# Performance work log

Measured on AMD Instinct MI355X. Metric: run time of the kernel, lower is better.

Reference implementation:

```python
import jax, jax.numpy as jnp
import numpy as np

N_ATOMS = 10000
N_PAIRS = 320000
C = 64        # channel width (pp_nodes[-1], ii_nodes[-1], pi_nodes[-1])
NB = 10       # n_basis
EPS = 1e-3    # torsion-boost epsilon


def setup_inputs() -> dict:
    key = jax.random.key(0)
    ks = jax.random.split(key, 24)
    f32 = jnp.float32

    def w(k, shp):
        return jax.random.normal(k, shp, f32) / np.float32(np.sqrt(shp[0]))

    ind_2 = jax.random.randint(ks[0], (N_PAIRS, 2), 0, N_ATOMS)
    p1 = jax.random.normal(ks[1], (N_ATOMS, C), f32)
    p3 = jax.random.normal(ks[2], (N_ATOMS, 3, C), f32)
    basis = jax.random.uniform(ks[3], (N_PAIRS, NB), dtype=f32)
    d3 = jax.random.normal(ks[4], (N_PAIRS, 3), f32)
    d3 = d3 / jnp.linalg.norm(d3, axis=-1, keepdims=True)  # unit bond directions
    fc_edge = jax.random.uniform(ks[5], (N_PAIRS, 1), dtype=f32)  # cutoff in [0,1]

    return {
        'ind_2': ind_2, 'p1': p1, 'p3': p3, 'basis': basis, 'd3': d3, 'fc_edge': fc_edge,
        'pp_pre_W1': w(ks[6], (C, C)), 'pp_pre_b1': jnp.zeros((C,), f32),
        'pp_pre_W2': w(ks[7], (C, C)), 'pp_pre_b2': jnp.zeros((C,), f32),
        'pi_W': w(ks[8], (2 * C, C * NB)), 'pi_b': jnp.zeros((C * NB,), f32),
        'ii_W': w(ks[9], (C, 2 * C)),
        'pp_post_W1': w(ks[10], (2 * C, C)), 'pp_post_W2': w(ks[11], (C, C)),
        'eq_pp_W': w(ks[12], (C, C)),
        'pp1_W1': w(ks[13], (2 * C, C)), 'pp1_b1': jnp.zeros((C,), f32),
        'pp1_W2': w(ks[14], (C, 2 * C)), 'pp1_b2': jnp.zeros((2 * C,), f32),
    }


def _gc_block(ind_2, p1, p3, basis, d3, fc_edge,
              pp_pre_W1, pp_pre_b1, pp_pre_W2, pp_pre_b2,
              pi_W, pi_b, ii_W, pp_post_W1, pp_post_W2,
              eq_pp_W, pp1_W1, pp1_b1, pp1_W2, pp1_b2):
    n_atoms = p1.shape[0]
    i = ind_2[:, 0]
    j = ind_2[:, 1]

    # ---- InvarLayer ----
    # pp_pre: FF [C,C], tanh, bias
    p1_in = jnp.tanh(jnp.tanh(p1 @ pp_pre_W1 + pp_pre_b1) @ pp_pre_W2 + pp_pre_b2)
    # PILayer: concat(p1[i], p1[j]) -> Dense(C*NB) -> contract with radial basis
    pair = jnp.concatenate([p1_in[i], p1_in[j]], axis=-1)            # (P, 2C)
    h = jnp.tanh(pair @ pi_W + pi_b).reshape(-1, C, NB)              # (P, C, NB)
    i_pair = jnp.einsum('pcb,pb->pc', h, basis)                      # (P, C)
    # ii: FF [2C] (doubled for n_props=2), tanh, no bias
    i_pair = jnp.tanh(i_pair @ ii_W)                                 # (P, 2C)
    # IP: scatter-add onto receiver atom i
    p1_scat = jax.ops.segment_sum(i_pair, i, num_segments=n_atoms)   # (N, 2C)
    # pp_post: FF [C,C], tanh, no bias
    p1_new = jnp.tanh(jnp.tanh(p1_scat @ pp_post_W1) @ pp_post_W2)   # (N, C)

    i1a, i1b = jnp.split(i_pair, 2, axis=-1)  # chunks; rank-3 branch uses i1s[1]

    # ---- torsion boost (compute_torsion_boost_t3) ----
    v = jax.ops.segment_sum(d3 * fc_edge, i, num_segments=n_atoms)   # (N, 3)
    v_i = v[i]
    proj = jnp.sum(v_i * d3, axis=-1, keepdims=True)
    w = v_i - proj * d3                                              # perpendicular part
    w2 = jnp.sum(w * w, axis=-1, keepdims=True)
    g_deg = w2 / (w2 + (10.0 * EPS) ** 2)
    t3 = w * jax.lax.rsqrt(w2 + EPS * EPS) * g_deg                   # (P, 3)
    tb_gate = g_deg * (fc_edge * fc_edge)                            # (P, 1)

    # ---- EquivarLayer ----
    gate = i1b[:, None, :]                                           # (P, 1, C)
    ix = p3[j] * gate + d3[:, :, None] * gate \
         + t3[:, :, None] * (i1b * tb_gate)[:, None, :]              # (P, 3, C)
    p3_new = jax.ops.segment_sum(ix, i, num_segments=n_atoms)        # (N, 3, C)
    p3_new = p3_new @ eq_pp_W                                        # PP: no bias, no act
    dotted = jnp.einsum('ixr,ixr->ir', p3_new, p3_new)               # (N, C)

    # ---- output PP + gating ----
    h2 = jnp.tanh(jnp.concatenate([p1_new, dotted], axis=-1) @ pp1_W1 + pp1_b1)
    h2 = jnp.tanh(h2 @ pp1_W2 + pp1_b2)                              # (N, 2C)
    g1, g3 = jnp.split(h2, 2, axis=-1)
    p1_out = g1                                                      # (N, C)
    p3_out = p3_new * g3[:, None, :]                                 # ScaleLayer
    return p1_out, p3_out


def reference(ind_2, p1, p3, basis, d3, fc_edge,
              pp_pre_W1, pp_pre_b1, pp_pre_W2, pp_pre_b2,
              pi_W, pi_b, ii_W, pp_post_W1, pp_post_W2,
              eq_pp_W, pp1_W1, pp1_b1, pp1_W2, pp1_b2):
    return _gc_block(ind_2, p1, p3, basis, d3, fc_edge,
                     pp_pre_W1, pp_pre_b1, pp_pre_W2, pp_pre_b2,
                     pi_W, pi_b, ii_W, pp_post_W1, pp_post_W2,
                     eq_pp_W, pp1_W1, pp1_b1, pp1_W2, pp1_b2)
```

## Files before the change

kernel.cpp:

```cpp
#include <hip/hip_runtime.h>
#include <hip/hip_bf16.h>

#define N_ATOMS 10000
#define N_PAIRS 320000
#define C_ 64
#define NB_ 10

typedef short bf16x8 __attribute__((ext_vector_type(8)));
typedef float f32x4 __attribute__((ext_vector_type(4)));

__device__ __forceinline__ float bf2f(__hip_bfloat16 x) { return __bfloat162float(x); }
__device__ __forceinline__ float ldf(const void* p, int i, int isf32) {
    return isf32 ? ((const float*)p)[i] : bf2f(((const __hip_bfloat16*)p)[i]);
}
__device__ __forceinline__ short f2bs(float x) {
    __hip_bfloat16 h = __float2bfloat16(x);
    return *reinterpret_cast<short*>(&h);
}
__device__ __forceinline__ float bs2f(unsigned short s) {
    return __uint_as_float(((unsigned)s) << 16);
}
__device__ __forceinline__ float tanh_fast(float x) {
    const float e = __expf(2.0f * x);
    return 1.0f - 2.0f * __builtin_amdgcn_rcpf(e + 1.0f);
}

#define W_PPREW1 0
#define W_PPREB1 4096
#define W_PPREW2 4160
#define W_PPREB2 8256
#define W_PIW    8320
#define W_PIB    90240
#define W_IIW    90880
#define W_PPOSTW1 99072
#define W_PPOSTW2 107264
#define W_EQW    111360
#define W_Q1W    115456
#define W_Q1B    123648
#define W_Q2W    123712
#define W_Q2B    131904
#define W_TOTAL  132032

__device__ __forceinline__ int probe_eval(const void* d3)
{
    float sf = 0.f, sb = 0.f;
    const float* f = (const float*)d3;
    const __hip_bfloat16* b = (const __hip_bfloat16*)d3;
    for (int r = 0; r < 4; r++) {
        float x = f[r*3], y = f[r*3+1], z = f[r*3+2];
        float n = x*x + y*y + z*z;
        sf += isfinite(n) ? fabsf(n - 1.f) : 1e30f;
        float xb = bf2f(b[r*3]), yb = bf2f(b[r*3+1]), zb = bf2f(b[r*3+2]);
        float nb = xb*xb + yb*yb + zb*zb;
        sb += isfinite(nb) ? fabsf(nb - 1.f) : 1e30f;
    }
    return (sf < sb) ? 1 : 0;
}

__global__ __launch_bounds__(256) void k_front(
    const void* __restrict__ d3, const void* __restrict__ fc,
    int* __restrict__ flag, const int* __restrict__ ind2,
    int* __restrict__ cnt, float* __restrict__ v,
    const void* s0, const void* s1, const void* s2, const void* s3,
    const void* s4, const void* s5, const void* s6, const void* s7,
    const void* s8, const void* s9, const void* s10, const void* s11,
    const void* s12, const void* s13,
    float* __restrict__ wbuf)
{
    __shared__ int fsh;
    if (threadIdx.x == 0) {
        const int fv = probe_eval(d3);
        fsh = fv;
        if (blockIdx.x == 0) *flag = fv;
    }
    __syncthreads();
    const int isf32 = fsh;
    if (blockIdx.x < 1250) {
        const int p = blockIdx.x * 256 + threadIdx.x;
        if (p >= N_PAIRS) return;
        const int ia = ind2[2 * p];
        atomicAdd(&cnt[ia], 1);
        const float f = ldf(fc, p, isf32);
        #pragma unroll
        for (int x = 0; x < 3; x++)
            atomicAdd(&v[ia * 3 + x], ldf(d3, 3 * p + x, isf32) * f);
        return;
    }
    const int idx = (blockIdx.x - 1250) * 256 + threadIdx.x;
    if (idx >= W_TOTAL) return;
    const int offw[15] = {W_PPREW1, W_PPREB1, W_PPREW2, W_PPREB2, W_PIW, W_PIB,
                          W_IIW, W_PPOSTW1, W_PPOSTW2, W_EQW, W_Q1W, W_Q1B,
                          W_Q2W, W_Q2B, W_TOTAL};
    const void* srcs[14] = {s0,s1,s2,s3,s4,s5,s6,s7,s8,s9,s10,s11,s12,s13};
    int t = 0;
    while (idx >= offw[t + 1]) t++;
    wbuf[idx] = ldf(srcs[t], idx - offw[t], isf32);
}

__global__ __launch_bounds__(256) void k_scan_wfrag(
    const int* __restrict__ cnt, int* __restrict__ offs, int* __restrict__ cur,
    const float* __restrict__ wbuf,
    short* __restrict__ w1Fh, short* __restrict__ w1Fl,
    short* __restrict__ w2Fh, short* __restrict__ w2Fl)
{
    if (blockIdx.x == 0) {
        if (!cnt) return;
        __shared__ int part[256];
        __shared__ int base[257];
        const int t = threadIdx.x;
        const int lo = t * 40, hi = (lo + 40 < N_ATOMS) ? lo + 40 : N_ATOMS;
        int s = 0;
        for (int b = lo; b < hi; b++) s += cnt[b];
        part[t] = s;
        __syncthreads();
        if (t == 0) {
            int run = 0;
            for (int i = 0; i < 256; i++) { base[i] = run; run += part[i]; }
            base[256] = run;
        }
        __syncthreads();
        int run = base[t];
        for (int b = lo; b < hi; b++) { offs[b] = run; cur[b] = run; run += cnt[b]; }
        if (t == 0) offs[N_ATOMS] = base[256];
        return;
    }
    const int b = blockIdx.x - 1;
    const int isW2 = b >= 16;
    const int idx = (b - (isW2 ? 16 : 0)) * 256 + threadIdx.x;
    const int j = idx & 7, lane = (idx >> 3) & 63, s2 = (idx >> 9) & 1, ct = idx >> 10;
    const int k = s2 * 32 + (lane >> 4) * 8 + j;
    const int col = ct * 16 + (lane & 15);
    const float wv = wbuf[(isW2 ? W_PPREW2 : W_PPREW1) + k * 64 + col];
    const short hs = f2bs(wv);
    short* dh = isW2 ? w2Fh : w1Fh;
    short* dl = isW2 ? w2Fl : w1Fl;
    dh[idx] = hs;
    dl[idx] = f2bs(wv - bs2f((unsigned short)hs));
}

__global__ __launch_bounds__(256) void k_prep_scatter(
    const float* __restrict__ wbuf,
    short* __restrict__ piWB2,
    short* __restrict__ iiWh, short* __restrict__ iiWl,
    const void* __restrict__ p1, const int* __restrict__ flagp,
    unsigned short* __restrict__ p1h, unsigned short* __restrict__ p1l,
    const int* __restrict__ ind2, int* __restrict__ cur, int* __restrict__ perm,
    const short* __restrict__ w1Fh, const short* __restrict__ w1Fl,
    const short* __restrict__ w2Fh, const short* __restrict__ w2Fl)
{
    __shared__ float hL[64 * 68];
    if (blockIdx.x >= 509) {
        const int p = (blockIdx.x - 509) * 256 + threadIdx.x;
        if (p < N_PAIRS) {
            const int pos = atomicAdd(&cur[ind2[2 * p]], 1);
            perm[pos] = p;
        }
        return;
    }
    if (blockIdx.x < 352) {
        int idx = blockIdx.x * 256 + threadIdx.x;
        if (idx < 81920) {
            const int j = idx & 7, lane = (idx >> 3) & 63, s = (idx >> 9) & 3, T = idx >> 11;
            const int k = s * 32 + (lane >> 4) * 8 + j;
            const int colp = T * 16 + (lane & 15);
            const int b = colp >> 6, c = colp & 63;
            const float v = wbuf[W_PIW + k * 640 + c * 10 + b];
            const short hs = f2bs(v);
            const int cc = idx >> 13, e = idx & 8191;
            piWB2[cc * 16384 + e] = hs;
            piWB2[cc * 16384 + 8192 + e] = f2bs(v - bs2f((unsigned short)hs));
            return;
        }
        idx -= 81920;
        if (idx < 8192) {
            const int j = idx & 7, lane = (idx >> 3) & 63, s2 = (idx >> 9) & 1, ct = idx >> 10;
            const int k = s2 * 32 + (lane >> 4) * 8 + j;
            const int col = ct * 16 + (lane & 15);
            const float wv = wbuf[W_IIW + k * 128 + col];
            const short hs = f2bs(wv);
            iiWh[idx] = hs;
            iiWl[idx] = f2bs(wv - bs2f((unsigned short)hs));
        }
        return;
    }
    const int isf32 = *flagp;
    const int t = threadIdx.x;
    const int lane = t & 63, w = t >> 6, lc = lane & 15, quad = lane >> 4;
    const int B0 = (blockIdx.x - 352) * 64;

    bf16x8 xh[2], xl[2];
    {
        const int a = B0 + w * 16 + lc;
        const int ar = (a < N_ATOMS) ? a : N_ATOMS - 1;
        #pragma unroll
        for (int s2 = 0; s2 < 2; s2++) {
            const int base = ar * 64 + s2 * 32 + quad * 8;
            #pragma unroll
            for (int j = 0; j < 8; j++) {
                const float x = ldf(p1, base + j, isf32);
                const short hs = f2bs(x);
                xh[s2][j] = hs;
                xl[s2][j] = f2bs(x - bs2f((unsigned short)hs));
            }
        }
    }
    #pragma unroll
    for (int tt = 0; tt < 4; tt++) {
        f32x4 acc = {0.f, 0.f, 0.f, 0.f};
        #pragma unroll
        for (int s2 = 0; s2 < 2; s2++) {
            bf16x8 bh = *(const bf16x8*)&w1Fh[((tt * 2 + s2) * 64 + lane) * 8];
            bf16x8 bl = *(const bf16x8*)&w1Fl[((tt * 2 + s2) * 64 + lane) * 8];
            acc = __builtin_amdgcn_mfma_f32_16x16x32_bf16(xh[s2], bh, acc, 0, 0, 0);
            acc = __builtin_amdgcn_mfma_f32_16x16x32_bf16(xl[s2], bh, acc, 0, 0, 0);
            acc = __builtin_amdgcn_mfma_f32_16x16x32_bf16(xh[s2], bl, acc, 0, 0, 0);
        }
        const int c = tt * 16 + lc;
        const float b1v = wbuf[W_PPREB1 + c];
        #pragma unroll
        for (int r = 0; r < 4; r++) {
            const int m = w * 16 + quad * 4 + r;
            hL[m * 68 + c] = tanh_fast(acc[r] + b1v);
        }
    }
    __syncthreads();
    bf16x8 hh[2], hl[2];
    {
        const int row = w * 16 + lc;
        #pragma unroll
        for (int s2 = 0; s2 < 2; s2++) {
            const float* pr = &hL[row * 68 + s2 * 32 + quad * 8];
            #pragma unroll
            for (int j = 0; j < 8; j++) {
                const float x = pr[j];
                const short hs = f2bs(x);
                hh[s2][j] = hs;
                hl[s2][j] = f2bs(x - bs2f((unsigned short)hs));
            }
        }
    }
    #pragma unroll
    for (int tt = 0; tt < 4; tt++) {
        f32x4 acc = {0.f, 0.f, 0.f, 0.f};
        #pragma unroll
        for (int s2 = 0; s2 < 2; s2++) {
            bf16x8 bh = *(const bf16x8*)&w2Fh[((tt * 2 + s2) * 64 + lane) * 8];
            bf16x8 bl = *(const bf16x8*)&w2Fl[((tt * 2 + s2) * 64 + lane) * 8];
            acc = __builtin_amdgcn_mfma_f32_16x16x32_bf16(hh[s2], bh, acc, 0, 0, 0);
            acc = __builtin_amdgcn_mfma_f32_16x16x32_bf16(hl[s2], bh, acc, 0, 0, 0);
            acc = __builtin_amdgcn_mfma_f32_16x16x32_bf16(hh[s2], bl, acc, 0, 0, 0);
        }
        const int c = tt * 16 + lc;
        const float b2v = wbuf[W_PPREB2 + c];
        #pragma unroll
        for (int r = 0; r < 4; r++) {
            const int m = w * 16 + quad * 4 + r;
            const int a = B0 + m;
            if (a < N_ATOMS) {
                const float f = tanh_fast(acc[r] + b2v);
                const short hs = f2bs(f);
                p1h[a * 64 + c] = (unsigned short)hs;
                p1l[a * 64 + c] = (unsigned short)f2bs(f - bs2f((unsigned short)hs));
            }
        }
    }
}

__global__ __launch_bounds__(256) void k_pairs_fused(
    const int* __restrict__ ind2, const void* __restrict__ basis,
    const void* __restrict__ d3, const void* __restrict__ fc,
    const int* __restrict__ perm,
    const void* __restrict__ p3,
    const float* __restrict__ wbuf,
    const short* __restrict__ piWB2,
    const short* __restrict__ iiWh, const short* __restrict__ iiWl,
    const unsigned short* __restrict__ p1h, const unsigned short* __restrict__ p1l,
    const int* __restrict__ flagp, const float* __restrict__ vglob,
    float* __restrict__ p1scat, float* __restrict__ p3acc)
{
    __shared__ __align__(16) char SH[33280];
    __shared__ float basisL[640];
    __shared__ float biasT[640];
    __shared__ int sIL[65], sJL[64];
    __shared__ float d3L[64][3], t3L[64][3], tbL[64];

    unsigned short* Bbuf = (unsigned short*)SH;
    float* preL = (float*)SH;
    float* ipL  = (float*)SH;

    const int t = threadIdx.x;
    const int bid = blockIdx.x;
    const int P0 = ((bid & 7) * 625 + (bid >> 3)) * 64;
    const int isf32 = *flagp;
    const int lane = t & 63;
    const int w = t >> 6;
    const int lc = lane & 15;
    const int quad = lane >> 4;

    if (t < 64) {
        const int p = perm[P0 + t];
        int2 ij = ((const int2*)ind2)[p];
        sIL[t] = ij.x; sJL[t] = ij.y;
        const float vi0 = vglob[ij.x * 3 + 0], vi1 = vglob[ij.x * 3 + 1], vi2 = vglob[ij.x * 3 + 2];
        const float d0 = ldf(d3, 3 * p + 0, isf32);
        const float d1 = ldf(d3, 3 * p + 1, isf32);
        const float d2 = ldf(d3, 3 * p + 2, isf32);
        d3L[t][0] = d0; d3L[t][1] = d1; d3L[t][2] = d2;
        const float proj = vi0 * d0 + vi1 * d1 + vi2 * d2;
        const float w0 = vi0 - proj * d0, w1 = vi1 - proj * d1, w2v = vi2 - proj * d2;
        const float w2 = w0 * w0 + w1 * w1 + w2v * w2v;
        const float g = w2 / (w2 + 1e-4f);
        const float rs = rsqrtf(w2 + 1e-6f);
        t3L[t][0] = w0 * rs * g; t3L[t][1] = w1 * rs * g; t3L[t][2] = w2v * rs * g;
        const float f = ldf(fc, p, isf32);
        tbL[t] = g * f * f;
    }
    if (t == 64) sIL[64] = -1;
    for (int e = t; e < 640; e += 256) {
        const int pm = e / 10, col = e - pm * 10;
        basisL[e] = ldf(basis, perm[P0 + pm] * 10 + col, isf32);
    }
    for (int e = t; e < 640; e += 256) biasT[e] = wbuf[W_PIB + (e & 63) * 10 + (e >> 6)];
    __syncthreads();

    bf16x8 ah[4], al[4];
    {
        const int ia = sIL[w * 16 + lc];
        const int ja = sJL[w * 16 + lc];
        #pragma unroll
        for (int s = 0; s < 4; s++) {
            const int atom = (s < 2) ? ia : ja;
            const int off = atom * 64 + (s & 1) * 32 + quad * 8;
            ah[s] = *(const bf16x8*)(p1h + off);
            al[s] = *(const bf16x8*)(p1l + off);
        }
    }

    float sr[4][4];
    #pragma unroll
    for (int r = 0; r < 4; r++)
        #pragma unroll
        for (int ph = 0; ph < 4; ph++) sr[r][ph] = 0.f;

    for (int cc = 0; cc < 10; cc++) {
        if (cc) __syncthreads();
        {
            const uint4* gsrc = (const uint4*)(piWB2 + cc * 16384);
            uint4* ldst = (uint4*)Bbuf;
            #pragma unroll
            for (int r = 0; r < 8; r++) ldst[r * 256 + t] = gsrc[r * 256 + t];
        }
        __syncthreads();
        #pragma unroll
        for (int tt = 0; tt < 4; tt++) {
            f32x4 acc = {0.f, 0.f, 0.f, 0.f};
            #pragma unroll
            for (int s = 0; s < 4; s++) {
                const int e = ((tt * 4 + s) * 64 + lane) * 8;
                bf16x8 bh = *(const bf16x8*)&Bbuf[e];
                bf16x8 bl = *(const bf16x8*)&Bbuf[8192 + e];
                acc = __builtin_amdgcn_mfma_f32_16x16x32_bf16(ah[s], bh, acc, 0, 0, 0);
                acc = __builtin_amdgcn_mfma_f32_16x16x32_bf16(al[s], bh, acc, 0, 0, 0);
                acc = __builtin_amdgcn_mfma_f32_16x16x32_bf16(ah[s], bl, acc, 0, 0, 0);
            }
            const float bias = biasT[cc * 64 + tt * 16 + lc];
            #pragma unroll
            for (int r = 0; r < 4; r++) {
                const int m = w * 16 + quad * 4 + r;
                const float h = tanh_fast(acc[r] + bias);
                sr[r][tt] += h * basisL[m * 10 + cc];
            }
        }
    }
    __syncthreads();

    #pragma unroll
    for (int r = 0; r < 4; r++)
        #pragma unroll
        for (int ph = 0; ph < 4; ph++)
            preL[(w * 16 + quad * 4 + r) * 68 + ph * 16 + lc] = sr[r][ph];
    __syncthreads();

    bf16x8 ah2[2], al2[2];
    {
        const int row = w * 16 + lc;
        #pragma unroll
        for (int s2 = 0; s2 < 2; s2++) {
            const float* pr2 = &preL[row * 68 + s2 * 32 + quad * 8];
            #pragma unroll
            for (int j = 0; j < 8; j++) {
                const float x = pr2[j];
                const short hs = f2bs(x);
                ah2[s2][j] = hs;
                al2[s2][j] = f2bs(x - bs2f((unsigned short)hs));
            }
        }
    }
    __syncthreads();

    float pv0[16];
    if (t < 192) {
        #pragma unroll
        for (int u = 0; u < 16; u++) pv0[u] = ldf(p3, sJL[u] * 192 + t, isf32);
    }

    #pragma unroll
    for (int ct = 0; ct < 8; ct++) {
        f32x4 acc = {0.f, 0.f, 0.f, 0.f};
        #pragma unroll
        for (int s2 = 0; s2 < 2; s2++) {
            bf16x8 bh = *(const bf16x8*)&iiWh[((ct * 2 + s2) * 64 + lane) * 8];
            bf16x8 bl = *(const bf16x8*)&iiWl[((ct * 2 + s2) * 64 + lane) * 8];
            acc = __builtin_amdgcn_mfma_f32_16x16x32_bf16(ah2[s2], bh, acc, 0, 0, 0);
            acc = __builtin_amdgcn_mfma_f32_16x16x32_bf16(al2[s2], bh, acc, 0, 0, 0);
            acc = __builtin_amdgcn_mfma_f32_16x16x32_bf16(ah2[s2], bl, acc, 0, 0, 0);
        }
        const int ch = ct * 16 + lc;
        #pragma unroll
        for (int r = 0; r < 4; r++) {
            const int m = w * 16 + quad * 4 + r;
            ipL[m * 130 + ch] = tanh_fast(acc[r]);
        }
    }
    __syncthreads();

    if (t < 192) {
        const int x = t >> 6, cc2 = t & 63;
        float acc = 0.f;
        #pragma unroll
        for (int blk = 0; blk < 4; blk++) {
            float pv[16];
            if (blk == 0) {
                #pragma unroll
                for (int u = 0; u < 16; u++) pv[u] = pv0[u];
            } else {
                #pragma unroll
                for (int u = 0; u < 16; u++)
                    pv[u] = ldf(p3, sJL[blk * 16 + u] * 192 + t, isf32);
            }
            #pragma unroll
            for (int u = 0; u < 16; u++) {
                const int m = blk * 16 + u;
                const float ipb = ipL[m * 130 + 64 + cc2];
                acc += (pv[u] + d3L[m][x]) * ipb + t3L[m][x] * (ipb * tbL[m]);
                if (sIL[m + 1] != sIL[m]) {
                    atomicAdd(&p3acc[(size_t)sIL[m] * 192 + t], acc);
                    acc = 0.f;
                }
            }
        }
    } else {
        const int ch0 = t - 192;
        float a0 = 0.f, a1 = 0.f;
        #pragma unroll 8
        for (int m = 0; m < 64; m++) {
            a0 += ipL[m * 130 + ch0];
            a1 += ipL[m * 130 + 64 + ch0];
            if (sIL[m + 1] != sIL[m]) {
                const size_t base = (size_t)sIL[m] * 128;
                atomicAdd(&p1scat[base + ch0], a0);
                atomicAdd(&p1scat[base + 64 + ch0], a1);
                a0 = 0.f; a1 = 0.f;
            }
        }
    }
}

__global__ __launch_bounds__(256) void k_pairs_atomic(
    const int* __restrict__ ind2, const void* __restrict__ basis,
    const void* __restrict__ d3, const void* __restrict__ fc,
    const void* __restrict__ p3,
    const float* __restrict__ wbuf,
    const short* __restrict__ piWB2,
    const short* __restrict__ iiWh, const short* __restrict__ iiWl,
    const unsigned short* __restrict__ p1h, const unsigned short* __restrict__ p1l,
    const int* __restrict__ flagp, const float* __restrict__ vglob,
    float* __restrict__ outA, float* __restrict__ outB)
{
    __shared__ __align__(16) unsigned short Bbuf[8192];
    __shared__ __align__(16) char SH[17408];
    __shared__ float basisL[640];
    __shared__ int sIL[64], sJL[64];
    __shared__ float d3L[64][3], t3L[64][3], tbL[64];

    float* preL = (float*)SH;
    float* i1bL = (float*)SH;

    const int t = threadIdx.x;
    const int P0 = blockIdx.x * 64;
    const int isf32 = *flagp;
    const int lane = t & 63;
    const int w = t >> 6;
    const int lc = lane & 15;
    const int quad = lane >> 4;

    if (t < 64) {
        int2 ij = ((const int2*)ind2)[P0 + t];
        sIL[t] = ij.x; sJL[t] = ij.y;
    }
    for (int e = t; e < 640; e += 256) basisL[e] = ldf(basis, P0 * 10 + e, isf32);
    __syncthreads();

    bf16x8 ah[4], al[4];
    {
        const int ia = sIL[w * 16 + lc];
        const int ja = sJL[w * 16 + lc];
        #pragma unroll
        for (int s = 0; s < 4; s++) {
            const int atom = (s < 2) ? ia : ja;
            const int off = atom * 64 + (s & 1) * 32 + quad * 8;
            ah[s] = *(const bf16x8*)(p1h + off);
            al[s] = *(const bf16x8*)(p1l + off);
        }
    }

    float sr[4][4];
    #pragma unroll
    for (int r = 0; r < 4; r++)
        #pragma unroll
        for (int ph = 0; ph < 4; ph++) sr[r][ph] = 0.f;

    for (int cc = 0; cc < 10; cc++) {
        f32x4 acc[4];
        #pragma unroll
        for (int tt = 0; tt < 4; tt++) acc[tt] = (f32x4){0.f, 0.f, 0.f, 0.f};

        __syncthreads();
        {
            const uint4* gsrc = (const uint4*)(piWB2 + cc * 16384);
            uint4* ldst = (uint4*)Bbuf;
            #pragma unroll
            for (int r = 0; r < 4; r++) ldst[r * 256 + t] = gsrc[r * 256 + t];
        }
        __syncthreads();
        #pragma unroll
        for (int tt = 0; tt < 4; tt++) {
            #pragma unroll
            for (int s = 0; s < 4; s++) {
                bf16x8 bfr = *(const bf16x8*)&Bbuf[((tt * 4 + s) * 64 + lane) * 8];
                acc[tt] = __builtin_amdgcn_mfma_f32_16x16x32_bf16(ah[s], bfr, acc[tt], 0, 0, 0);
                acc[tt] = __builtin_amdgcn_mfma_f32_16x16x32_bf16(al[s], bfr, acc[tt], 0, 0, 0);
            }
        }
        __syncthreads();
        {
            const uint4* gsrc = (const uint4*)(piWB2 + cc * 16384 + 8192);
            uint4* ldst = (uint4*)Bbuf;
            #pragma unroll
            for (int r = 0; r < 4; r++) ldst[r * 256 + t] = gsrc[r * 256 + t];
        }
        __syncthreads();
        #pragma unroll
        for (int tt = 0; tt < 4; tt++) {
            #pragma unroll
            for (int s = 0; s < 4; s++) {
                bf16x8 bfr = *(const bf16x8*)&Bbuf[((tt * 4 + s) * 64 + lane) * 8];
                acc[tt] = __builtin_amdgcn_mfma_f32_16x16x32_bf16(ah[s], bfr, acc[tt], 0, 0, 0);
            }
            const int c = tt * 16 + lc;
            const float bias = wbuf[W_PIB + c * 10 + cc];
            #pragma unroll
            for (int r = 0; r < 4; r++) {
                const int m = w * 16 + quad * 4 + r;
                const float h = tanh_fast(acc[tt][r] + bias);
                sr[r][tt] += h * basisL[m * 10 + cc];
            }
        }
    }

    #pragma unroll
    for (int r = 0; r < 4; r++)
        #pragma unroll
        for (int ph = 0; ph < 4; ph++)
            preL[(w * 16 + quad * 4 + r) * 68 + ph * 16 + lc] = sr[r][ph];
    __syncthreads();

    bf16x8 ah2[2], al2[2];
    {
        const int row = w * 16 + lc;
        #pragma unroll
        for (int s2 = 0; s2 < 2; s2++) {
            const float* pr2 = &preL[row * 68 + s2 * 32 + quad * 8];
            #pragma unroll
            for (int j = 0; j < 8; j++) {
                const float x = pr2[j];
                const short hs = f2bs(x);
                ah2[s2][j] = hs;
                al2[s2][j] = f2bs(x - bs2f((unsigned short)hs));
            }
        }
    }
    __syncthreads();

    #pragma unroll
    for (int ct = 0; ct < 8; ct++) {
        f32x4 acc = {0.f, 0.f, 0.f, 0.f};
        #pragma unroll
        for (int s2 = 0; s2 < 2; s2++) {
            bf16x8 bh = *(const bf16x8*)&iiWh[((ct * 2 + s2) * 64 + lane) * 8];
            bf16x8 bl = *(const bf16x8*)&iiWl[((ct * 2 + s2) * 64 + lane) * 8];
            acc = __builtin_amdgcn_mfma_f32_16x16x32_bf16(ah2[s2], bh, acc, 0, 0, 0);
            acc = __builtin_amdgcn_mfma_f32_16x16x32_bf16(al2[s2], bh, acc, 0, 0, 0);
            acc = __builtin_amdgcn_mfma_f32_16x16x32_bf16(ah2[s2], bl, acc, 0, 0, 0);
        }
        const int ch = ct * 16 + lc;
        #pragma unroll
        for (int r = 0; r < 4; r++) {
            const int m = w * 16 + quad * 4 + r;
            const float val = tanh_fast(acc[r]);
            atomicAdd(&outA[(size_t)sIL[m] * 128 + ch], val);
            if (ch >= 64) i1bL[m * 64 + (ch - 64)] = val;
        }
    }

    __syncthreads();
    if (t < 64) {
        const int m = t;
        const int ia = sIL[m];
        const float vi0 = vglob[ia * 3 + 0], vi1 = vglob[ia * 3 + 1], vi2 = vglob[ia * 3 + 2];
        const float d0 = ldf(d3, (P0 + m) * 3 + 0, isf32);
        const float d1 = ldf(d3, (P0 + m) * 3 + 1, isf32);
        const float d2 = ldf(d3, (P0 + m) * 3 + 2, isf32);
        d3L[m][0] = d0; d3L[m][1] = d1; d3L[m][2] = d2;
        const float proj = vi0 * d0 + vi1 * d1 + vi2 * d2;
        const float w0 = vi0 - proj * d0, w1 = vi1 - proj * d1, w2v = vi2 - proj * d2;
        const float w2 = w0 * w0 + w1 * w1 + w2v * w2v;
        const float g = w2 / (w2 + 1e-4f);
        const float rs = rsqrtf(w2 + 1e-6f);
        t3L[m][0] = w0 * rs * g; t3L[m][1] = w1 * rs * g; t3L[m][2] = w2v * rs * g;
        const float f = ldf(fc, P0 + m, isf32);
        tbL[m] = g * f * f;
    }
    __syncthreads();
    const int c = lane;
    #pragma unroll 4
    for (int mm = 0; mm < 16; mm++) {
        const int m = w * 16 + mm;
        const float bv = i1bL[m * 64 + c];
        const float coef = bv * tbL[m];
        #pragma unroll
        for (int x = 0; x < 3; x++) {
            const float p3v = ldf(p3, sJL[m] * 192 + x * 64 + c, isf32);
            atomicAdd(&outB[(size_t)sIL[m] * 192 + x * 64 + c],
                      p3v * bv + d3L[m][x] * bv + t3L[m][x] * coef);
        }
    }
}

__global__ __launch_bounds__(256) void k_final(
    const float* __restrict__ p1scat, const float* __restrict__ p3acc,
    const float* __restrict__ wbuf, const int* __restrict__ flagp,
    void* __restrict__ out)
{
    const float* ppW1 = wbuf + W_PPOSTW1;
    const float* ppW2 = wbuf + W_PPOSTW2;
    const float* eqW  = wbuf + W_EQW;
    const float* q1W  = wbuf + W_Q1W;
    const float* q1b  = wbuf + W_Q1B;
    const float* q2W  = wbuf + W_Q2W;
    const float* q2b  = wbuf + W_Q2B;
    const int isf32 = *flagp;

    __shared__ float s1[4][128];
    __shared__ float hA[4][64];
    __shared__ float cat[4][128];
    __shared__ float p3a[4][192];
    const int t = threadIdx.x;
    const int slot = t >> 6, c = t & 63;
    const int atom = blockIdx.x * 4 + slot;

    s1[slot][c]        = p1scat[atom * 128 + c];
    s1[slot][64 + c]   = p1scat[atom * 128 + 64 + c];
    p3a[slot][c]       = p3acc[atom * 192 + c];
    p3a[slot][64 + c]  = p3acc[atom * 192 + 64 + c];
    p3a[slot][128 + c] = p3acc[atom * 192 + 128 + c];
    __syncthreads();

    float acc = 0.f;
    for (int k = 0; k < 128; k++) acc += s1[slot][k] * ppW1[k * 64 + c];
    hA[slot][c] = tanh_fast(acc);
    __syncthreads();
    acc = 0.f;
    for (int k = 0; k < 64; k++) acc += hA[slot][k] * ppW2[k * 64 + c];
    cat[slot][c] = tanh_fast(acc);

    float pn[3];
    float dot = 0.f;
    #pragma unroll
    for (int x = 0; x < 3; x++) {
        float a = 0.f;
        for (int k = 0; k < 64; k++) a += p3a[slot][x * 64 + k] * eqW[k * 64 + c];
        pn[x] = a;
        dot += a * a;
    }
    cat[slot][64 + c] = dot;
    __syncthreads();

    acc = q1b[c];
    for (int k = 0; k < 128; k++) acc += cat[slot][k] * q1W[k * 64 + c];
    __syncthreads();
    hA[slot][c] = tanh_fast(acc);
    __syncthreads();

    float g1acc = q2b[c], g3acc = q2b[c + 64];
    for (int k = 0; k < 64; k++) {
        const float hv = hA[slot][k];
        g1acc += hv * q2W[k * 128 + c];
        g3acc += hv * q2W[k * 128 + c + 64];
    }
    const float g1 = tanh_fast(g1acc);
    const float g3 = tanh_fast(g3acc);
    if (isf32) {
        float* p1o = (float*)out;
        float* p3o = p1o + 640000;
        p1o[atom * 64 + c] = g1;
        #pragma unroll
        for (int x = 0; x < 3; x++) p3o[atom * 192 + x * 64 + c] = pn[x] * g3;
    } else {
        __hip_bfloat16* p1o = (__hip_bfloat16*)out;
        __hip_bfloat16* p3o = p1o + 640000;
        p1o[atom * 64 + c] = __float2bfloat16(g1);
        #pragma unroll
        for (int x = 0; x < 3; x++) p3o[atom * 192 + x * 64 + c] = __float2bfloat16(pn[x] * g3);
    }
}

extern "C" void kernel_launch(void* const* d_in, const int* in_sizes, int n_in,
                              void* d_out, int out_size, void* d_ws, size_t ws_size,
                              hipStream_t stream)
{
    const int* ind2 = (const int*)d_in[0];
    const void* p1    = d_in[1];
    const void* p3    = d_in[2];
    const void* basis = d_in[3];
    const void* d3    = d_in[4];
    const void* fc    = d_in[5];

    char* W = (char*)d_ws;
    float* wbuf  = (float*)(W + 0);
    short* piWB2 = (short*)(W + 528128);
    short* iiWh  = (short*)(W + 1183488);
    short* iiWl  = (short*)(W + 1199872);
    unsigned short* p1h = (unsigned short*)(W + 1216256);
    unsigned short* p1l = (unsigned short*)(W + 2496256);
    int* flag = (int*)(W + 3776256);
    short* w1Fh = (short*)(W + 3776320);
    short* w1Fl = (short*)(W + 3784512);
    short* w2Fh = (short*)(W + 3792704);
    short* w2Fl = (short*)(W + 3800896);

    const int fused = (ws_size >= 18129216ULL) ? 1 : 0;

    if (fused) {
        int* offs     = (int*)(W + 3809088);
        int* cur      = (int*)(W + 3849216);
        int* perm     = (int*)(W + 3889216);
        int* cnt      = (int*)(W + 5169216);
        float* v      = (float*)(W + 5209216);
        float* p1scat = (float*)(W + 5329216);
        float* p3acc  = (float*)(W + 10449216);

        hipMemsetAsync(cnt, 0, 40000 + 120000 + 5120000 + 7680000, stream);
        k_front<<<1766, 256, 0, stream>>>(d3, fc, flag, ind2, cnt, v,
            d_in[6], d_in[7], d_in[8], d_in[9], d_in[10], d_in[11], d_in[12],
            d_in[13], d_in[14], d_in[15], d_in[16], d_in[17], d_in[18], d_in[19],
            wbuf);
        k_scan_wfrag<<<33, 256, 0, stream>>>(cnt, offs, cur, wbuf,
                                             w1Fh, w1Fl, w2Fh, w2Fl);
        k_prep_scatter<<<1759, 256, 0, stream>>>(wbuf, piWB2, iiWh, iiWl, p1, flag,
                                                 p1h, p1l, ind2, cur, perm,
                                                 w1Fh, w1Fl, w2Fh, w2Fl);
        k_pairs_fused<<<5000, 256, 0, stream>>>(ind2, basis, d3, fc, perm, p3,
                                                wbuf, piWB2, iiWh, iiWl,
                                                p1h, p1l, flag, v, p1scat, p3acc);
        k_final<<<2500, 256, 0, stream>>>(p1scat, p3acc, wbuf, flag, d_out);
    } else {
        int* cnt      = (int*)(W + 3809088);
        float* v      = (float*)(W + 3849088);
        float* p1scat = (float*)(W + 3969088);
        float* p3acc  = (float*)(W + 9089088);

        hipMemsetAsync(cnt, 0, 40000 + 120000 + 5120000 + 7680000, stream);
        k_front<<<1766, 256, 0, stream>>>(d3, fc, flag, ind2, cnt, v,
            d_in[6], d_in[7], d_in[8], d_in[9], d_in[10], d_in[11], d_in[12],
            d_in[13], d_in[14], d_in[15], d_in[16], d_in[17], d_in[18], d_in[19],
            wbuf);
        k_scan_wfrag<<<33, 256, 0, stream>>>(nullptr, nullptr, nullptr, wbuf,
                                             w1Fh, w1Fl, w2Fh, w2Fl);
        k_prep_scatter<<<509, 256, 0, stream>>>(wbuf, piWB2, iiWh, iiWl, p1, flag,
                                                p1h, p1l, nullptr, nullptr, nullptr,
                                                w1Fh, w1Fl, w2Fh, w2Fl);
        k_pairs_atomic<<<5000, 256, 0, stream>>>(ind2, basis, d3, fc, p3,
                                                 wbuf, piWB2, iiWh, iiWl,
                                                 p1h, p1l, flag, v,
                                                 p1scat, p3acc);
        k_final<<<2500, 256, 0, stream>>>(p1scat, p3acc, wbuf, flag, d_out);
    }
}
```

Before: 522.8 us.

## Rewrite per-atom output MLP as split-bf16 MFMA kernel with prepacked weight fragments

Replaces the scalar per-atom final kernel, which handled 4 atoms per block, with an MFMA kernel that handles 64 atoms per block. Every dense layer (pp_post, eq_pp, pp1) uses hi/lo bf16 splitting with three MFMAs to stay close to fp32 accuracy. The scan kernel gains extra blocks that pack those weights into MFMA fragment layout, and workspace offsets are shifted to make room. The aim is to cut the FMA-bound cost of the final stage, at the price of three MFMAs per product, a larger prep launch and a bigger workspace requirement.

```diff
diff --git a/kernel.cpp b/kernel.cpp
--- a/kernel.cpp
+++ b/kernel.cpp
@@ -101,16 +101,22 @@
     const int* __restrict__ cnt, int* __restrict__ offs, int* __restrict__ cur,
     const float* __restrict__ wbuf,
     short* __restrict__ w1Fh, short* __restrict__ w1Fl,
-    short* __restrict__ w2Fh, short* __restrict__ w2Fl)
+    short* __restrict__ w2Fh, short* __restrict__ w2Fl,
+    short* __restrict__ pAh, short* __restrict__ pAl,
+    short* __restrict__ pBh, short* __restrict__ pBl,
+    short* __restrict__ pEh, short* __restrict__ pEl,
+    short* __restrict__ pQ1h, short* __restrict__ pQ1l,
+    short* __restrict__ pQ2h, short* __restrict__ pQ2l)
 {
-    if (blockIdx.x == 0) {
+    const int b = blockIdx.x;
+    if (b == 0) {
         if (!cnt) return;
         __shared__ int part[256];
         __shared__ int base[257];
         const int t = threadIdx.x;
         const int lo = t * 40, hi = (lo + 40 < N_ATOMS) ? lo + 40 : N_ATOMS;
         int s = 0;
-        for (int b = lo; b < hi; b++) s += cnt[b];
+        for (int bb = lo; bb < hi; bb++) s += cnt[bb];
         part[t] = s;
         __syncthreads();
         if (t == 0) {
@@ -120,22 +126,63 @@
         }
         __syncthreads();
         int run = base[t];
-        for (int b = lo; b < hi; b++) { offs[b] = run; cur[b] = run; run += cnt[b]; }
+        for (int bb = lo; bb < hi; bb++) { offs[bb] = run; cur[bb] = run; run += cnt[bb]; }
         if (t == 0) offs[N_ATOMS] = base[256];
         return;
     }
-    const int b = blockIdx.x - 1;
-    const int isW2 = b >= 16;
-    const int idx = (b - (isW2 ? 16 : 0)) * 256 + threadIdx.x;
-    const int j = idx & 7, lane = (idx >> 3) & 63, s2 = (idx >> 9) & 1, ct = idx >> 10;
-    const int k = s2 * 32 + (lane >> 4) * 8 + j;
-    const int col = ct * 16 + (lane & 15);
-    const float wv = wbuf[(isW2 ? W_PPREW2 : W_PPREW1) + k * 64 + col];
-    const short hs = f2bs(wv);
-    short* dh = isW2 ? w2Fh : w1Fh;
-    short* dl = isW2 ? w2Fl : w1Fl;
-    dh[idx] = hs;
-    dl[idx] = f2bs(wv - bs2f((unsigned short)hs));
+    if (b < 33) {
+        const int bb = b - 1;
+        const int isW2 = bb >= 16;
+        const int idx = (bb - (isW2 ? 16 : 0)) * 256 + threadIdx.x;
+        const int j = idx & 7, lane = (idx >> 3) & 63, s2 = (idx >> 9) & 1, ct = idx >> 10;
+        const int k = s2 * 32 + (lane >> 4) * 8 + j;
+        const int col = ct * 16 + (lane & 15);
+        const float wv = wbuf[(isW2 ? W_PPREW2 : W_PPREW1) + k * 64 + col];
+        const short hs = f2bs(wv);
+        short* dh = isW2 ? w2Fh : w1Fh;
+        short* dl = isW2 ? w2Fl : w1Fl;
+        dh[idx] = hs;
+        dl[idx] = f2bs(wv - bs2f((unsigned short)hs));
+        return;
+    }
+    if (b < 65 || (b >= 97 && b < 129)) {
+        const int isQ1 = (b >= 97);
+        const int idx = (b - (isQ1 ? 97 : 33)) * 256 + threadIdx.x;
+        const int j = idx & 7, lane = (idx >> 3) & 63, s = (idx >> 9) & 3, tt = idx >> 11;
+        const int k = s * 32 + (lane >> 4) * 8 + j;
+        const int col = tt * 16 + (lane & 15);
+        const float wv = wbuf[(isQ1 ? W_Q1W : W_PPOSTW1) + k * 64 + col];
+        const short hs = f2bs(wv);
+        short* dh = isQ1 ? pQ1h : pAh;
+        short* dl = isQ1 ? pQ1l : pAl;
+        dh[idx] = hs;
+        dl[idx] = f2bs(wv - bs2f((unsigned short)hs));
+        return;
+    }
+    if (b < 97) {
+        const int isE = b >= 81;
+        const int idx = (b - (isE ? 81 : 65)) * 256 + threadIdx.x;
+        const int j = idx & 7, lane = (idx >> 3) & 63, s2 = (idx >> 9) & 1, ct = idx >> 10;
+        const int k = s2 * 32 + (lane >> 4) * 8 + j;
+        const int col = ct * 16 + (lane & 15);
+        const float wv = wbuf[(isE ? W_EQW : W_PPOSTW2) + k * 64 + col];
+        const short hs = f2bs(wv);
+        short* dh = isE ? pEh : pBh;
+        short* dl = isE ? pEl : pBl;
+        dh[idx] = hs;
+        dl[idx] = f2bs(wv - bs2f((unsigned short)hs));
+        return;
+    }
+    {
+        const int idx = (b - 129) * 256 + threadIdx.x;
+        const int j = idx & 7, lane = (idx >> 3) & 63, s2 = (idx >> 9) & 1, ct = idx >> 10;
+        const int k = s2 * 32 + (lane >> 4) * 8 + j;
+        const int col = ct * 16 + (lane & 15);
+        const float wv = wbuf[W_Q2W + k * 128 + col];
+        const short hs = f2bs(wv);
+        pQ2h[idx] = hs;
+        pQ2l[idx] = f2bs(wv - bs2f((unsigned short)hs));
+    }
 }
 
 __global__ __launch_bounds__(256) void k_prep_scatter(
@@ -647,81 +694,217 @@
     }
 }
 
-__global__ __launch_bounds__(256) void k_final(
+__global__ __launch_bounds__(256) void k_final_mfma(
     const float* __restrict__ p1scat, const float* __restrict__ p3acc,
     const float* __restrict__ wbuf, const int* __restrict__ flagp,
+    const short* __restrict__ pAh, const short* __restrict__ pAl,
+    const short* __restrict__ pBh, const short* __restrict__ pBl,
+    const short* __restrict__ pEh, const short* __restrict__ pEl,
+    const short* __restrict__ pQ1h, const short* __restrict__ pQ1l,
+    const short* __restrict__ pQ2h, const short* __restrict__ pQ2l,
     void* __restrict__ out)
 {
-    const float* ppW1 = wbuf + W_PPOSTW1;
-    const float* ppW2 = wbuf + W_PPOSTW2;
-    const float* eqW  = wbuf + W_EQW;
-    const float* q1W  = wbuf + W_Q1W;
-    const float* q1b  = wbuf + W_Q1B;
-    const float* q2W  = wbuf + W_Q2W;
-    const float* q2b  = wbuf + W_Q2B;
+    __shared__ float hL[64 * 68];
+    __shared__ float catL[64 * 132];
     const int isf32 = *flagp;
-
-    __shared__ float s1[4][128];
-    __shared__ float hA[4][64];
-    __shared__ float cat[4][128];
-    __shared__ float p3a[4][192];
     const int t = threadIdx.x;
-    const int slot = t >> 6, c = t & 63;
-    const int atom = blockIdx.x * 4 + slot;
-
-    s1[slot][c]        = p1scat[atom * 128 + c];
-    s1[slot][64 + c]   = p1scat[atom * 128 + 64 + c];
-    p3a[slot][c]       = p3acc[atom * 192 + c];
-    p3a[slot][64 + c]  = p3acc[atom * 192 + 64 + c];
-    p3a[slot][128 + c] = p3acc[atom * 192 + 128 + c];
-    __syncthreads();
-
-    float acc = 0.f;
-    for (int k = 0; k < 128; k++) acc += s1[slot][k] * ppW1[k * 64 + c];
-    hA[slot][c] = tanh_fast(acc);
-    __syncthreads();
-    acc = 0.f;
-    for (int k = 0; k < 64; k++) acc += hA[slot][k] * ppW2[k * 64 + c];
-    cat[slot][c] = tanh_fast(acc);
-
-    float pn[3];
-    float dot = 0.f;
+    const int lane = t & 63, w = t >> 6, lc = lane & 15, quad = lane >> 4;
+    const int B0 = blockIdx.x * 64;
+    const int arow = B0 + w * 16 + lc;
+    const int ar = (arow < N_ATOMS) ? arow : N_ATOMS - 1;
+
+    {
+        bf16x8 xh[4], xl[4];
+        #pragma unroll
+        for (int s = 0; s < 4; s++) {
+            const float* src = p1scat + (size_t)ar * 128 + s * 32 + quad * 8;
+            #pragma unroll
+            for (int j = 0; j < 8; j++) {
+                const float x = src[j];
+                const short hs = f2bs(x);
+                xh[s][j] = hs;
+                xl[s][j] = f2bs(x - bs2f((unsigned short)hs));
+            }
+        }
+        #pragma unroll
+        for (int tt = 0; tt < 4; tt++) {
+            f32x4 acc = {0.f, 0.f, 0.f, 0.f};
+            #pragma unroll
+            for (int s = 0; s < 4; s++) {
+                bf16x8 bh = *(const bf16x8*)&pAh[((tt * 4 + s) * 64 + lane) * 8];
+                bf16x8 bl = *(const bf16x8*)&pAl[((tt * 4 + s) * 64 + lane) * 8];
+                acc = __builtin_amdgcn_mfma_f32_16x16x32_bf16(xh[s], bh, acc, 0, 0, 0);
+                acc = __builtin_amdgcn_mfma_f32_16x16x32_bf16(xl[s], bh, acc, 0, 0, 0);
+                acc = __builtin_amdgcn_mfma_f32_16x16x32_bf16(xh[s], bl, acc, 0, 0, 0);
+            }
+            const int c = tt * 16 + lc;
+            #pragma unroll
+            for (int r = 0; r < 4; r++)
+                hL[(w * 16 + quad * 4 + r) * 68 + c] = tanh_fast(acc[r]);
+        }
+    }
+    __syncthreads();
+
+    {
+        bf16x8 hh[2], hl[2];
+        const int row = w * 16 + lc;
+        #pragma unroll
+        for (int s2 = 0; s2 < 2; s2++) {
+            const float* pr = &hL[row * 68 + s2 * 32 + quad * 8];
+            #pragma unroll
+            for (int j = 0; j < 8; j++) {
+                const float x = pr[j];
+                const short hs = f2bs(x);
+                hh[s2][j] = hs;
+                hl[s2][j] = f2bs(x - bs2f((unsigned short)hs));
+            }
+        }
+        #pragma unroll
+        for (int tt = 0; tt < 4; tt++) {
+            f32x4 acc = {0.f, 0.f, 0.f, 0.f};
+            #pragma unroll
+            for (int s2 = 0; s2 < 2; s2++) {
+                bf16x8 bh = *(const bf16x8*)&pBh[((tt * 2 + s2) * 64 + lane) * 8];
+                bf16x8 bl = *(const bf16x8*)&pBl[((tt * 2 + s2) * 64 + lane) * 8];
+                acc = __builtin_amdgcn_mfma_f32_16x16x32_bf16(hh[s2], bh, acc, 0, 0, 0);
+                acc = __builtin_amdgcn_mfma_f32_16x16x32_bf16(hl[s2], bh, acc, 0, 0, 0);
+                acc = __builtin_amdgcn_mfma_f32_16x16x32_bf16(hh[s2], bl, acc, 0, 0, 0);
+            }
+            const int c = tt * 16 + lc;
+            #pragma unroll
+            for (int r = 0; r < 4; r++)
+                catL[(w * 16 + quad * 4 + r) * 132 + c] = tanh_fast(acc[r]);
+        }
+    }
+
+    float pn[3][4][4];
     #pragma unroll
     for (int x = 0; x < 3; x++) {
-        float a = 0.f;
-        for (int k = 0; k < 64; k++) a += p3a[slot][x * 64 + k] * eqW[k * 64 + c];
-        pn[x] = a;
-        dot += a * a;
-    }
-    cat[slot][64 + c] = dot;
-    __syncthreads();
-
-    acc = q1b[c];
-    for (int k = 0; k < 128; k++) acc += cat[slot][k] * q1W[k * 64 + c];
-    __syncthreads();
-    hA[slot][c] = tanh_fast(acc);
-    __syncthreads();
-
-    float g1acc = q2b[c], g3acc = q2b[c + 64];
-    for (int k = 0; k < 64; k++) {
-        const float hv = hA[slot][k];
-        g1acc += hv * q2W[k * 128 + c];
-        g3acc += hv * q2W[k * 128 + c + 64];
-    }
-    const float g1 = tanh_fast(g1acc);
-    const float g3 = tanh_fast(g3acc);
-    if (isf32) {
-        float* p1o = (float*)out;
-        float* p3o = p1o + 640000;
-        p1o[atom * 64 + c] = g1;
-        #pragma unroll
-        for (int x = 0; x < 3; x++) p3o[atom * 192 + x * 64 + c] = pn[x] * g3;
-    } else {
-        __hip_bfloat16* p1o = (__hip_bfloat16*)out;
-        __hip_bfloat16* p3o = p1o + 640000;
-        p1o[atom * 64 + c] = __float2bfloat16(g1);
-        #pragma unroll
-        for (int x = 0; x < 3; x++) p3o[atom * 192 + x * 64 + c] = __float2bfloat16(pn[x] * g3);
+        bf16x8 ph[2], pl[2];
+        #pragma unroll
+        for (int s2 = 0; s2 < 2; s2++) {
+            const float* src = p3acc + (size_t)ar * 192 + x * 64 + s2 * 32 + quad * 8;
+            #pragma unroll
+            for (int j = 0; j < 8; j++) {
+                const float xv = src[j];
+                const short hs = f2bs(xv);
+                ph[s2][j] = hs;
+                pl[s2][j] = f2bs(xv - bs2f((unsigned short)hs));
+            }
+        }
+        #pragma unroll
+        for (int tt = 0; tt < 4; tt++) {
+            f32x4 acc = {0.f, 0.f, 0.f, 0.f};
+            #pragma unroll
+            for (int s2 = 0; s2 < 2; s2++) {
+                bf16x8 bh = *(const bf16x8*)&pEh[((tt * 2 + s2) * 64 + lane) * 8];
+                bf16x8 bl = *(const bf16x8*)&pEl[((tt * 2 + s2) * 64 + lane) * 8];
+                acc = __builtin_amdgcn_mfma_f32_16x16x32_bf16(ph[s2], bh, acc, 0, 0, 0);
+                acc = __builtin_amdgcn_mfma_f32_16x16x32_bf16(pl[s2], bh, acc, 0, 0, 0);
+                acc = __builtin_amdgcn_mfma_f32_16x16x32_bf16(ph[s2], bl, acc, 0, 0, 0);
+            }
+            #pragma unroll
+            for (int r = 0; r < 4; r++) pn[x][tt][r] = acc[r];
+        }
+    }
+    #pragma unroll
+    for (int tt = 0; tt < 4; tt++) {
+        const int c = tt * 16 + lc;
+        #pragma unroll
+        for (int r = 0; r < 4; r++) {
+            const float d = pn[0][tt][r] * pn[0][tt][r]
+                          + pn[1][tt][r] * pn[1][tt][r]
+                          + pn[2][tt][r] * pn[2][tt][r];
+            catL[(w * 16 + quad * 4 + r) * 132 + 64 + c] = d;
+        }
+    }
+    __syncthreads();
+
+    {
+        bf16x8 ch[4], cl[4];
+        const int row = w * 16 + lc;
+        #pragma unroll
+        for (int s = 0; s < 4; s++) {
+            const float* pr = &catL[row * 132 + s * 32 + quad * 8];
+            #pragma unroll
+            for (int j = 0; j < 8; j++) {
+                const float x = pr[j];
+                const short hs = f2bs(x);
+                ch[s][j] = hs;
+                cl[s][j] = f2bs(x - bs2f((unsigned short)hs));
+            }
+        }
+        #pragma unroll
+        for (int tt = 0; tt < 4; tt++) {
+            f32x4 acc = {0.f, 0.f, 0.f, 0.f};
+            #pragma unroll
+            for (int s = 0; s < 4; s++) {
+                bf16x8 bh = *(const bf16x8*)&pQ1h[((tt * 4 + s) * 64 + lane) * 8];
+                bf16x8 bl = *(const bf16x8*)&pQ1l[((tt * 4 + s) * 64 + lane) * 8];
+                acc = __builtin_amdgcn_mfma_f32_16x16x32_bf16(ch[s], bh, acc, 0, 0, 0);
+                acc = __builtin_amdgcn_mfma_f32_16x16x32_bf16(cl[s], bh, acc, 0, 0, 0);
+                acc = __builtin_amdgcn_mfma_f32_16x16x32_bf16(ch[s], bl, acc, 0, 0, 0);
+            }
+            const int c = tt * 16 + lc;
+            const float b1v = wbuf[W_Q1B + c];
+            #pragma unroll
+            for (int r = 0; r < 4; r++)
+                hL[(w * 16 + quad * 4 + r) * 68 + c] = tanh_fast(acc[r] + b1v);
+        }
+    }
+    __syncthreads();
+
+    bf16x8 gh[2], gl[2];
+    {
+        const int row = w * 16 + lc;
+        #pragma unroll
+        for (int s2 = 0; s2 < 2; s2++) {
+            const float* pr = &hL[row * 68 + s2 * 32 + quad * 8];
+            #pragma unroll
+            for (int j = 0; j < 8; j++) {
+                const float x = pr[j];
+                const short hs = f2bs(x);
+                gh[s2][j] = hs;
+                gl[s2][j] = f2bs(x - bs2f((unsigned short)hs));
+            }
+        }
+    }
+    float* p1o32 = (float*)out;
+    float* p3o32 = p1o32 + 640000;
+    __hip_bfloat16* p1o16 = (__hip_bfloat16*)out;
+    __hip_bfloat16* p3o16 = p1o16 + 640000;
+    #pragma unroll
+    for (int ct = 0; ct < 8; ct++) {
+        f32x4 acc = {0.f, 0.f, 0.f, 0.f};
+        #pragma unroll
+        for (int s2 = 0; s2 < 2; s2++) {
+            bf16x8 bh = *(const bf16x8*)&pQ2h[((ct * 2 + s2) * 64 + lane) * 8];
+            bf16x8 bl = *(const bf16x8*)&pQ2l[((ct * 2 + s2) * 64 + lane) * 8];
+            acc = __builtin_amdgcn_mfma_f32_16x16x32_bf16(gh[s2], bh, acc, 0, 0, 0);
+            acc = __builtin_amdgcn_mfma_f32_16x16x32_bf16(gl[s2], bh, acc, 0, 0, 0);
+            acc = __builtin_amdgcn_mfma_f32_16x16x32_bf16(gh[s2], bl, acc, 0, 0, 0);
+        }
+        const int col = ct * 16 + lc;
+        const float qb = wbuf[W_Q2B + col];
+        #pragma unroll
+        for (int r = 0; r < 4; r++) {
+            const int m = w * 16 + quad * 4 + r;
+            const int a = B0 + m;
+            if (a >= N_ATOMS) continue;
+            const float val = tanh_fast(acc[r] + qb);
+            if (ct < 4) {
+                if (isf32) p1o32[a * 64 + col] = val;
+                else       p1o16[a * 64 + col] = __float2bfloat16(val);
+            } else {
+                const int c2 = col - 64;
+                #pragma unroll
+                for (int x = 0; x < 3; x++) {
+                    const float pv = pn[x][ct - 4][r] * val;
+                    if (isf32) p3o32[a * 192 + x * 64 + c2] = pv;
+                    else       p3o16[a * 192 + x * 64 + c2] = __float2bfloat16(pv);
+                }
+            }
+        }
     }
 }
 
@@ -748,45 +931,61 @@
     short* w1Fl = (short*)(W + 3784512);
     short* w2Fh = (short*)(W + 3792704);
     short* w2Fl = (short*)(W + 3800896);
-
-    const int fused = (ws_size >= 18129216ULL) ? 1 : 0;
+    short* pAh  = (short*)(W + 3809088);
+    short* pAl  = (short*)(W + 3825472);
+    short* pBh  = (short*)(W + 3841856);
+    short* pBl  = (short*)(W + 3850048);
+    short* pEh  = (short*)(W + 3858240);
+    short* pEl  = (short*)(W + 3866432);
+    short* pQ1h = (short*)(W + 3874624);
+    short* pQ1l = (short*)(W + 3891008);
+    short* pQ2h = (short*)(W + 3907392);
+    short* pQ2l = (short*)(W + 3923776);
+
+    const int fused = (ws_size >= 18260224ULL) ? 1 : 0;
 
     if (fused) {
-        int* offs     = (int*)(W + 3809088);
-        int* cur      = (int*)(W + 3849216);
-        int* perm     = (int*)(W + 3889216);
-        int* cnt      = (int*)(W + 5169216);
-        float* v      = (float*)(W + 5209216);
-        float* p1scat = (float*)(W + 5329216);
-        float* p3acc  = (float*)(W + 10449216);
+        int* offs     = (int*)(W + 3940160);
+        int* cur      = (int*)(W + 3980224);
+        int* perm     = (int*)(W + 4020224);
+        int* cnt      = (int*)(W + 5300224);
+        float* v      = (float*)(W + 5340224);
+        float* p1scat = (float*)(W + 5460224);
+        float* p3acc  = (float*)(W + 10580224);
 
         hipMemsetAsync(cnt, 0, 40000 + 120000 + 5120000 + 7680000, stream);
         k_front<<<1766, 256, 0, stream>>>(d3, fc, flag, ind2, cnt, v,
             d_in[6], d_in[7], d_in[8], d_in[9], d_in[10], d_in[11], d_in[12],
             d_in[13], d_in[14], d_in[15], d_in[16], d_in[17], d_in[18], d_in[19],
             wbuf);
-        k_scan_wfrag<<<33, 256, 0, stream>>>(cnt, offs, cur, wbuf,
-                                             w1Fh, w1Fl, w2Fh, w2Fl);
+        k_scan_wfrag<<<161, 256, 0, stream>>>(cnt, offs, cur, wbuf,
+                                              w1Fh, w1Fl, w2Fh, w2Fl,
+                                              pAh, pAl, pBh, pBl, pEh, pEl,
+                                              pQ1h, pQ1l, pQ2h, pQ2l);
         k_prep_scatter<<<1759, 256, 0, stream>>>(wbuf, piWB2, iiWh, iiWl, p1, flag,
                                                  p1h, p1l, ind2, cur, perm,
                                                  w1Fh, w1Fl, w2Fh, w2Fl);
         k_pairs_fused<<<5000, 256, 0, stream>>>(ind2, basis, d3, fc, perm, p3,
                                                 wbuf, piWB2, iiWh, iiWl,
                                                 p1h, p1l, flag, v, p1scat, p3acc);
-        k_final<<<2500, 256, 0, stream>>>(p1scat, p3acc, wbuf, flag, d_out);
+        k_final_mfma<<<157, 256, 0, stream>>>(p1scat, p3acc, wbuf, flag,
+                                              pAh, pAl, pBh, pBl, pEh, pEl,
+                                              pQ1h, pQ1l, pQ2h, pQ2l, d_out);
     } else {
-        int* cnt      = (int*)(W + 3809088);
-        float* v      = (float*)(W + 3849088);
-        float* p1scat = (float*)(W + 3969088);
-        float* p3acc  = (float*)(W + 9089088);
+        int* cnt      = (int*)(W + 3940160);
+        float* v      = (float*)(W + 3980160);
+        float* p1scat = (float*)(W + 4100160);
+        float* p3acc  = (float*)(W + 9220160);
 
         hipMemsetAsync(cnt, 0, 40000 + 120000 + 5120000 + 7680000, stream);
         k_front<<<1766, 256, 0, stream>>>(d3, fc, flag, ind2, cnt, v,
             d_in[6], d_in[7], d_in[8], d_in[9], d_in[10], d_in[11], d_in[12],
             d_in[13], d_in[14], d_in[15], d_in[16], d_in[17], d_in[18], d_in[19],
             wbuf);
-        k_scan_wfrag<<<33, 256, 0, stream>>>(nullptr, nullptr, nullptr, wbuf,
-                                             w1Fh, w1Fl, w2Fh, w2Fl);
+        k_scan_wfrag<<<161, 256, 0, stream>>>(nullptr, nullptr, nullptr, wbuf,
+                                              w1Fh, w1Fl, w2Fh, w2Fl,
+                                              pAh, pAl, pBh, pBl, pEh, pEl,
+                                              pQ1h, pQ1l, pQ2h, pQ2l);
         k_prep_scatter<<<509, 256, 0, stream>>>(wbuf, piWB2, iiWh, iiWl, p1, flag,
                                                 p1h, p1l, nullptr, nullptr, nullptr,
                                                 w1Fh, w1Fl, w2Fh, w2Fl);
@@ -794,6 +993,8 @@
                                                  wbuf, piWB2, iiWh, iiWl,
                                                  p1h, p1l, flag, v,
                                                  p1scat, p3acc);
-        k_final<<<2500, 256, 0, stream>>>(p1scat, p3acc, wbuf, flag, d_out);
-    }
-}
+        k_final_mfma<<<157, 256, 0, stream>>>(p1scat, p3acc, wbuf, flag,
+                                              pAh, pAl, pBh, pBl, pEh, pEl,
+                                              pQ1h, pQ1l, pQ2h, pQ2l, d_out);
+    }
+}
```

Result: faster. 484.9 us (-7.3%).
